# Kernel optimization log

Measured on AMD Instinct MI355X. Metric: run time of the kernel, lower is better.

## Reference

```python
import jax, jax.numpy as jnp
import numpy as np

E, T, D, N_RBF, N_SBF = 262144, 1048576, 128, 6, 42


def setup_inputs() -> dict:
    key = jax.random.key(0)
    ks = jax.random.split(key, 24)
    s = 0.05
    inp = {
        "m_ji": jax.random.normal(ks[0], (E, D), jnp.float32),
        "e_rbf": jax.random.normal(ks[1], (E, N_RBF), jnp.float32),
        "a_sbf": jax.random.normal(ks[2], (T, N_SBF), jnp.float32),
        "nbr_list": jax.random.randint(ks[3], (E, 2), 0, 65536),
        "kj_idx": jax.random.randint(ks[4], (T,), 0, E),
        "ji_idx": jax.random.randint(ks[5], (T,), 0, E),
        # edge branch params
        "We": jax.random.normal(ks[6], (N_RBF, D), jnp.float32) * s,
        "W_e1": jax.random.normal(ks[7], (D, D), jnp.float32) * s,
        "b_e1": jnp.zeros((D,), jnp.float32),
        "W_e2": jax.random.normal(ks[8], (D, D), jnp.float32) * s,
        "b_e2": jnp.zeros((D,), jnp.float32),
        "W_e3": jax.random.normal(ks[9], (D, D), jnp.float32) * s,
        "b_e3": jnp.zeros((D,), jnp.float32),
        "W_e4": jax.random.normal(ks[10], (D, D), jnp.float32) * s,
        # angle branch params
        "Wa": jax.random.normal(ks[11], (N_SBF, D), jnp.float32) * s,
        "W_a1": jax.random.normal(ks[12], (D, D), jnp.float32) * s,
        "b_a1": jnp.zeros((D,), jnp.float32),
        "W_a2": jax.random.normal(ks[13], (D, D), jnp.float32) * s,
        "b_a2": jnp.zeros((D,), jnp.float32),
        "W_a3": jax.random.normal(ks[14], (D, D), jnp.float32) * s,
        "b_a3": jnp.zeros((D,), jnp.float32),
        "W_a4": jax.random.normal(ks[15], (D, D), jnp.float32) * s,
    }
    return inp


def _mlp(x, W1, b1, W2, b2, W3, b3, W4):
    x = jax.nn.silu(x @ W1 + b1)
    x = jax.nn.silu(x @ W2 + b2)
    x = jax.nn.silu(x @ W3 + b3)
    return x @ W4


def reference(m_ji, e_rbf, a_sbf, nbr_list, kj_idx, ji_idx,
              We, W_e1, b_e1, W_e2, b_e2, W_e3, b_e3, W_e4,
              Wa, W_a1, b_a1, W_a2, b_a2, W_a3, b_a3, W_a4):
    # edge branch: project rbf to embed dim, gate by edge messages  [E, D]
    edge_feats = _mlp((e_rbf @ We) * m_ji, W_e1, b_e1, W_e2, b_e2, W_e3, b_e3, W_e4)
    # angle branch: project sbf, gate by triplet-gathered message sum  [T, D]
    angle_gate = m_ji[kj_idx] + m_ji[ji_idx]
    angle_feats = _mlp((a_sbf @ Wa) * angle_gate, W_a1, b_a1, W_a2, b_a2, W_a3, b_a3, W_a4)
    return (edge_feats, angle_feats)
```

## Files before the change

kernel.cpp:

```cpp
#include <hip/hip_runtime.h>
#include <stdint.h>

typedef __attribute__((ext_vector_type(8))) short bf16x8;
typedef __attribute__((ext_vector_type(4))) float f32x4;
typedef __attribute__((ext_vector_type(8))) unsigned short us8;
typedef __bf16 bf16v2 __attribute__((ext_vector_type(2)));

#define T_CNT 1048576
#define E_CNT 262144

static __device__ __forceinline__ unsigned short f2bf_u(float f) {
  __bf16 h = (__bf16)f;
  return __builtin_bit_cast(unsigned short, h);
}
static __device__ __forceinline__ uint32_t pack2bf(float a, float b) {
  bf16v2 t; t[0] = (__bf16)a; t[1] = (__bf16)b;
  return __builtin_bit_cast(uint32_t, t);
}
static __device__ __forceinline__ float silu_f(float v) {
  float e = __builtin_amdgcn_exp2f(v * -1.44269504088896341f);
  return v * __builtin_amdgcn_rcpf(1.0f + e);
}
static __device__ __forceinline__ bf16x8 frag8(f32x4 a, f32x4 b) {
  union { bf16x8 v; uint32_t u[4]; } r;
  r.u[0] = pack2bf(a[0], a[1]); r.u[1] = pack2bf(a[2], a[3]);
  r.u[2] = pack2bf(b[0], b[1]); r.u[3] = pack2bf(b[2], b[3]);
  return r.v;
}

static __device__ __forceinline__ void mlp4(
    char* __restrict__ xbA, char* __restrict__ xbB,
    const char* __restrict__ wt4,
    const float* __restrict__ b1, const float* __restrict__ b2,
    const float* __restrict__ b3, float* __restrict__ outT,
    int l15, int q, int w, int rs)
{
  const int cb = w * 32;
  #pragma unroll
  for (int L = 0; L < 4; ++L) {
    const char* src = (L & 1) ? xbB : xbA;
    char* dst = (L & 1) ? xbA : xbB;
    bf16x8 wf[2][4];
    #pragma unroll
    for (int ct = 0; ct < 2; ++ct)
      #pragma unroll
      for (int ks = 0; ks < 4; ++ks)
        wf[ct][ks] = *(const bf16x8*)(wt4 + (L << 15) + (((w * 2 + ct) * 4 + ks) << 10) + (l15 | (q << 4)) * 16);
    if (L < 3) {
      const float* bp = (L == 0) ? b1 : (L == 1) ? b2 : b3;
      f32x4 bv0 = *(const f32x4*)(bp + cb + q * 4);
      f32x4 bv1 = *(const f32x4*)(bp + cb + 16 + q * 4);
      #pragma unroll
      for (int rg = 0; rg < 2; ++rg) {
        const int row = rg * 16 + l15;
        f32x4 acc0 = {0.f,0.f,0.f,0.f}, acc1 = {0.f,0.f,0.f,0.f};
        #pragma unroll
        for (int ks = 0; ks < 4; ++ks) {
          bf16x8 xf = *(const bf16x8*)(src + ((row * 256 + ks * 64 + q * 16) ^ rs));
          acc0 = __builtin_amdgcn_mfma_f32_16x16x32_bf16(wf[0][ks], xf, acc0, 0, 0, 0);
          acc1 = __builtin_amdgcn_mfma_f32_16x16x32_bf16(wf[1][ks], xf, acc1, 0, 0, 0);
        }
        uint2 u0, u1;
        u0.x = pack2bf(silu_f(acc0[0] + bv0[0]), silu_f(acc0[1] + bv0[1]));
        u0.y = pack2bf(silu_f(acc0[2] + bv0[2]), silu_f(acc0[3] + bv0[3]));
        u1.x = pack2bf(silu_f(acc1[0] + bv1[0]), silu_f(acc1[1] + bv1[1]));
        u1.y = pack2bf(silu_f(acc1[2] + bv1[2]), silu_f(acc1[3] + bv1[3]));
        *(uint2*)(dst + ((row * 256 + w * 64 + q * 8) ^ rs)) = u0;
        *(uint2*)(dst + ((row * 256 + w * 64 + 32 + q * 8) ^ rs)) = u1;
      }
      __syncthreads();
    } else {
      #pragma unroll
      for (int rg = 0; rg < 2; ++rg) {
        const int row = rg * 16 + l15;
        f32x4 acc0 = {0.f,0.f,0.f,0.f}, acc1 = {0.f,0.f,0.f,0.f};
        #pragma unroll
        for (int ks = 0; ks < 4; ++ks) {
          bf16x8 xf = *(const bf16x8*)(src + ((row * 256 + ks * 64 + q * 16) ^ rs));
          acc0 = __builtin_amdgcn_mfma_f32_16x16x32_bf16(wf[0][ks], xf, acc0, 0, 0, 0);
          acc1 = __builtin_amdgcn_mfma_f32_16x16x32_bf16(wf[1][ks], xf, acc1, 0, 0, 0);
        }
        float* op = outT + (size_t)row * 128 + cb + q * 4;
        __builtin_nontemporal_store(acc0, (f32x4*)(op));
        __builtin_nontemporal_store(acc1, (f32x4*)(op + 16));
      }
    }
  }
}

__global__ __launch_bounds__(256, 4) void angle_kernel(
    const float* __restrict__ m_ji, const float* __restrict__ a_sbf,
    const int* __restrict__ kj, const int* __restrict__ ji,
    const float* __restrict__ b1, const float* __restrict__ b2,
    const float* __restrict__ b3,
    const char* __restrict__ wt4, const char* __restrict__ waT,
    float* __restrict__ out)
{
  __shared__ __align__(16) char xbA[8192];
  __shared__ __align__(16) char xbB[8192];
  const int tid = threadIdx.x, lane = tid & 63, w = tid >> 6;
  const int l15 = lane & 15, q = lane >> 4;
  const int rs = (l15 & 7) << 4;
  const size_t tb = (size_t)blockIdx.x * 32;
  const int cb = w * 32;

  bf16x8 wa[2][2];
  #pragma unroll
  for (int ct = 0; ct < 2; ++ct)
    #pragma unroll
    for (int ks = 0; ks < 2; ++ks)
      wa[ct][ks] = *(const bf16x8*)(waT + (((w * 2 + ct) * 2 + ks) << 10) + lane * 16);

  int ikj[2], iji[2];
  #pragma unroll
  for (int g = 0; g < 2; ++g) {
    ikj[g] = kj[tb + g * 16 + l15];
    iji[g] = ji[tb + g * 16 + l15];
  }
  f32x4 pk[2][2], pj[2][2];
  #pragma unroll
  for (int g = 0; g < 2; ++g) {
    const float* bk = m_ji + (size_t)ikj[g] * 128 + cb + q * 4;
    const float* bj = m_ji + (size_t)iji[g] * 128 + cb + q * 4;
    pk[g][0] = *(const f32x4*)(bk);
    pk[g][1] = *(const f32x4*)(bk + 16);
    pj[g][0] = *(const f32x4*)(bj);
    pj[g][1] = *(const f32x4*)(bj + 16);
  }

  #pragma unroll
  for (int rg = 0; rg < 2; ++rg) {
    const int row = rg * 16 + l15;
    const float* ap = a_sbf + (tb + row) * 42;
    f32x4 a0 = *(const f32x4*)(ap + q * 8);
    f32x4 a1 = *(const f32x4*)(ap + q * 8 + 4);
    f32x4 c0 = {0.f,0.f,0.f,0.f}, c1 = {0.f,0.f,0.f,0.f};
    if (q == 0) { c0 = *(const f32x4*)(ap + 32); c1 = *(const f32x4*)(ap + 36); }
    else if (q == 1) { float2 t = *(const float2*)(ap + 40); c0[0] = t.x; c0[1] = t.y; }
    bf16x8 f0 = frag8(a0, a1);
    bf16x8 f1 = frag8(c0, c1);
    f32x4 acc0 = {0.f,0.f,0.f,0.f}, acc1 = {0.f,0.f,0.f,0.f};
    acc0 = __builtin_amdgcn_mfma_f32_16x16x32_bf16(wa[0][0], f0, acc0, 0, 0, 0);
    acc0 = __builtin_amdgcn_mfma_f32_16x16x32_bf16(wa[0][1], f1, acc0, 0, 0, 0);
    acc1 = __builtin_amdgcn_mfma_f32_16x16x32_bf16(wa[1][0], f0, acc1, 0, 0, 0);
    acc1 = __builtin_amdgcn_mfma_f32_16x16x32_bf16(wa[1][1], f1, acc1, 0, 0, 0);
    f32x4 g0 = pk[rg][0] + pj[rg][0];
    f32x4 g1 = pk[rg][1] + pj[rg][1];
    uint2 u0, u1;
    u0.x = pack2bf(acc0[0] * g0[0], acc0[1] * g0[1]);
    u0.y = pack2bf(acc0[2] * g0[2], acc0[3] * g0[3]);
    u1.x = pack2bf(acc1[0] * g1[0], acc1[1] * g1[1]);
    u1.y = pack2bf(acc1[2] * g1[2], acc1[3] * g1[3]);
    *(uint2*)(xbA + ((row * 256 + w * 64 + q * 8) ^ rs)) = u0;
    *(uint2*)(xbA + ((row * 256 + w * 64 + 32 + q * 8) ^ rs)) = u1;
  }
  __syncthreads();

  mlp4(xbA, xbB, wt4, b1, b2, b3, out + tb * 128, l15, q, w, rs);
}

__global__ __launch_bounds__(256, 4) void edge_kernel(
    const float* __restrict__ m_ji, const float* __restrict__ e_rbf,
    const float* __restrict__ b1, const float* __restrict__ b2,
    const float* __restrict__ b3,
    const char* __restrict__ wt4, const char* __restrict__ weT,
    float* __restrict__ out)
{
  __shared__ __align__(16) char xbA[8192];
  __shared__ __align__(16) char xbB[8192];
  const int tid = threadIdx.x, lane = tid & 63, w = tid >> 6;
  const int l15 = lane & 15, q = lane >> 4;
  const int rs = (l15 & 7) << 4;
  const size_t tb = (size_t)blockIdx.x * 32;
  const int cb = w * 32;

  bf16x8 we[2];
  #pragma unroll
  for (int ct = 0; ct < 2; ++ct)
    we[ct] = *(const bf16x8*)(weT + ((w * 2 + ct) << 10) + lane * 16);

  f32x4 mr[2][2];
  #pragma unroll
  for (int g = 0; g < 2; ++g) {
    const float* bm = m_ji + (tb + g * 16 + l15) * 128 + cb + q * 4;
    mr[g][0] = *(const f32x4*)(bm);
    mr[g][1] = *(const f32x4*)(bm + 16);
  }

  #pragma unroll
  for (int rg = 0; rg < 2; ++rg) {
    const int row = rg * 16 + l15;
    const float* ep = e_rbf + (tb + row) * 6;
    f32x4 a0 = {0.f,0.f,0.f,0.f}, a1 = {0.f,0.f,0.f,0.f};
    if (q == 0) {
      a0 = *(const f32x4*)(ep);
      float2 t = *(const float2*)(ep + 4);
      a1[0] = t.x; a1[1] = t.y;
    }
    bf16x8 ef = frag8(a0, a1);
    f32x4 acc0 = {0.f,0.f,0.f,0.f}, acc1 = {0.f,0.f,0.f,0.f};
    acc0 = __builtin_amdgcn_mfma_f32_16x16x32_bf16(we[0], ef, acc0, 0, 0, 0);
    acc1 = __builtin_amdgcn_mfma_f32_16x16x32_bf16(we[1], ef, acc1, 0, 0, 0);
    f32x4 g0 = mr[rg][0];
    f32x4 g1 = mr[rg][1];
    uint2 u0, u1;
    u0.x = pack2bf(acc0[0] * g0[0], acc0[1] * g0[1]);
    u0.y = pack2bf(acc0[2] * g0[2], acc0[3] * g0[3]);
    u1.x = pack2bf(acc1[0] * g1[0], acc1[1] * g1[1]);
    u1.y = pack2bf(acc1[2] * g1[2], acc1[3] * g1[3]);
    *(uint2*)(xbA + ((row * 256 + w * 64 + q * 8) ^ rs)) = u0;
    *(uint2*)(xbA + ((row * 256 + w * 64 + 32 + q * 8) ^ rs)) = u1;
  }
  __syncthreads();

  mlp4(xbA, xbB, wt4, b1, b2, b3, out + tb * 128, l15, q, w, rs);
}

__global__ void prep_kernel(
    const float* __restrict__ W0, const float* __restrict__ W1,
    const float* __restrict__ W2, const float* __restrict__ W3,
    const float* __restrict__ W4, const float* __restrict__ W5,
    const float* __restrict__ W6, const float* __restrict__ W7,
    const float* __restrict__ Wa, const float* __restrict__ We,
    char* __restrict__ ws)
{
  const int gid = blockIdx.x * 256 + threadIdx.x;
  const int lane = gid & 63;
  const int l15 = lane & 15, q = lane >> 4;
  if (gid < 16384) {
    const int mat = gid >> 11;
    const int ctks = (gid & 2047) >> 6;
    const int n = (ctks >> 2) * 16 + l15;
    const int k0 = (ctks & 3) * 32 + q * 8;
    const float* W;
    switch (mat) {
      case 0: W = W0; break; case 1: W = W1; break;
      case 2: W = W2; break; case 3: W = W3; break;
      case 4: W = W4; break; case 5: W = W5; break;
      case 6: W = W6; break; default: W = W7; break;
    }
    us8 v;
    #pragma unroll
    for (int j = 0; j < 8; ++j) v[j] = f2bf_u(W[(size_t)(k0 + j) * 128 + n]);
    *(us8*)(ws + mat * 32768 + ctks * 1024 + lane * 16) = v;
  } else if (gid < 17408) {
    const int g = gid - 16384;
    const int ctks = g >> 6;
    const int n = (ctks >> 1) * 16 + l15;
    const int k0 = (ctks & 1) * 32 + q * 8;
    us8 v;
    #pragma unroll
    for (int j = 0; j < 8; ++j) {
      const int k = k0 + j;
      v[j] = (k < 42) ? f2bf_u(Wa[(size_t)k * 128 + n]) : (unsigned short)0;
    }
    *(us8*)(ws + 262144 + ctks * 1024 + lane * 16) = v;
  } else if (gid < 17920) {
    const int g = gid - 17408;
    const int ct = g >> 6;
    const int n = ct * 16 + l15;
    const int k0 = q * 8;
    us8 v;
    #pragma unroll
    for (int j = 0; j < 8; ++j) {
      const int k = k0 + j;
      v[j] = (k < 6) ? f2bf_u(We[(size_t)k * 128 + n]) : (unsigned short)0;
    }
    *(us8*)(ws + 278528 + ct * 1024 + lane * 16) = v;
  }
}

extern "C" void kernel_launch(void* const* d_in, const int* in_sizes, int n_in,
                              void* d_out, int out_size, void* d_ws, size_t ws_size,
                              hipStream_t stream) {
  (void)in_sizes; (void)n_in; (void)out_size; (void)ws_size;
  const float* m_ji  = (const float*)d_in[0];
  const float* e_rbf = (const float*)d_in[1];
  const float* a_sbf = (const float*)d_in[2];
  const int*   kj    = (const int*)d_in[4];
  const int*   ji    = (const int*)d_in[5];
  const float* We    = (const float*)d_in[6];
  const float* We1   = (const float*)d_in[7];
  const float* be1   = (const float*)d_in[8];
  const float* We2   = (const float*)d_in[9];
  const float* be2   = (const float*)d_in[10];
  const float* We3   = (const float*)d_in[11];
  const float* be3   = (const float*)d_in[12];
  const float* We4   = (const float*)d_in[13];
  const float* Wa    = (const float*)d_in[14];
  const float* Wa1   = (const float*)d_in[15];
  const float* ba1   = (const float*)d_in[16];
  const float* Wa2   = (const float*)d_in[17];
  const float* ba2   = (const float*)d_in[18];
  const float* Wa3   = (const float*)d_in[19];
  const float* ba3   = (const float*)d_in[20];
  const float* Wa4   = (const float*)d_in[21];
  char* ws = (char*)d_ws;
  float* out = (float*)d_out;
  float* out_a = out + (size_t)E_CNT * 128;

  prep_kernel<<<70, 256, 0, stream>>>(
      We1, We2, We3, We4, Wa1, Wa2, Wa3, Wa4, Wa, We, ws);
  edge_kernel<<<E_CNT / 32, 256, 0, stream>>>(
      m_ji, e_rbf, be1, be2, be3, ws, ws + 278528, out);
  angle_kernel<<<T_CNT / 32, 256, 0, stream>>>(
      m_ji, a_sbf, kj, ji, ba1, ba2, ba3, ws + 131072, ws + 262144, out_a);
}
```

Baseline: 584.0 us.

## Double rows per block, stage final output through LDS for coalesced stores

Each block now handles 64 rows instead of 32, so every weight fragment loaded from global memory is reused across twice as many rows, and there are half as many blocks. The last layer's fp32 results are written into a swizzled 32KB shared buffer and then streamed out as fully contiguous 16-byte nontemporal stores. The gather loads for m_ji are software-pipelined two row-groups ahead, and a_sbf is read with scalar nontemporal loads. In exchange, shared memory per block grows to 32KB, register pressure rises from holding accumulators for four row groups, and the scalar a_sbf loads may issue more memory instructions.

```diff
diff --git a/kernel.cpp b/kernel.cpp
--- a/kernel.cpp
+++ b/kernel.cpp
@@ -29,15 +29,18 @@
 }
 
 static __device__ __forceinline__ void mlp4(
-    char* __restrict__ xbA, char* __restrict__ xbB,
-    const char* __restrict__ wt4,
+    char* __restrict__ xb, const char* __restrict__ wt4,
     const float* __restrict__ b1, const float* __restrict__ b2,
     const float* __restrict__ b3, float* __restrict__ outT,
-    int l15, int q, int w, int rs)
+    int tid, int l15, int q, int w, int rs)
 {
+  char* xbA = xb;
+  char* xbB = xb + 16384;
   const int cb = w * 32;
-  #pragma unroll
-  for (int L = 0; L < 4; ++L) {
+  const int lane16 = (l15 | (q << 4)) * 16;
+
+  #pragma unroll
+  for (int L = 0; L < 3; ++L) {
     const char* src = (L & 1) ? xbB : xbA;
     char* dst = (L & 1) ? xbA : xbB;
     bf16x8 wf[2][4];
@@ -45,45 +48,71 @@
     for (int ct = 0; ct < 2; ++ct)
       #pragma unroll
       for (int ks = 0; ks < 4; ++ks)
-        wf[ct][ks] = *(const bf16x8*)(wt4 + (L << 15) + (((w * 2 + ct) * 4 + ks) << 10) + (l15 | (q << 4)) * 16);
-    if (L < 3) {
-      const float* bp = (L == 0) ? b1 : (L == 1) ? b2 : b3;
-      f32x4 bv0 = *(const f32x4*)(bp + cb + q * 4);
-      f32x4 bv1 = *(const f32x4*)(bp + cb + 16 + q * 4);
-      #pragma unroll
-      for (int rg = 0; rg < 2; ++rg) {
-        const int row = rg * 16 + l15;
-        f32x4 acc0 = {0.f,0.f,0.f,0.f}, acc1 = {0.f,0.f,0.f,0.f};
-        #pragma unroll
-        for (int ks = 0; ks < 4; ++ks) {
-          bf16x8 xf = *(const bf16x8*)(src + ((row * 256 + ks * 64 + q * 16) ^ rs));
-          acc0 = __builtin_amdgcn_mfma_f32_16x16x32_bf16(wf[0][ks], xf, acc0, 0, 0, 0);
-          acc1 = __builtin_amdgcn_mfma_f32_16x16x32_bf16(wf[1][ks], xf, acc1, 0, 0, 0);
-        }
-        uint2 u0, u1;
-        u0.x = pack2bf(silu_f(acc0[0] + bv0[0]), silu_f(acc0[1] + bv0[1]));
-        u0.y = pack2bf(silu_f(acc0[2] + bv0[2]), silu_f(acc0[3] + bv0[3]));
-        u1.x = pack2bf(silu_f(acc1[0] + bv1[0]), silu_f(acc1[1] + bv1[1]));
-        u1.y = pack2bf(silu_f(acc1[2] + bv1[2]), silu_f(acc1[3] + bv1[3]));
-        *(uint2*)(dst + ((row * 256 + w * 64 + q * 8) ^ rs)) = u0;
-        *(uint2*)(dst + ((row * 256 + w * 64 + 32 + q * 8) ^ rs)) = u1;
+        wf[ct][ks] = *(const bf16x8*)(wt4 + (L << 15) + (((w * 2 + ct) * 4 + ks) << 10) + lane16);
+    const float* bp = (L == 0) ? b1 : (L == 1) ? b2 : b3;
+    f32x4 bv0 = *(const f32x4*)(bp + cb + q * 4);
+    f32x4 bv1 = *(const f32x4*)(bp + cb + 16 + q * 4);
+    #pragma unroll
+    for (int rg = 0; rg < 4; ++rg) {
+      const int row = rg * 16 + l15;
+      f32x4 acc0 = {0.f,0.f,0.f,0.f}, acc1 = {0.f,0.f,0.f,0.f};
+      #pragma unroll
+      for (int ks = 0; ks < 4; ++ks) {
+        bf16x8 xf = *(const bf16x8*)(src + ((row * 256 + ks * 64 + q * 16) ^ rs));
+        acc0 = __builtin_amdgcn_mfma_f32_16x16x32_bf16(wf[0][ks], xf, acc0, 0, 0, 0);
+        acc1 = __builtin_amdgcn_mfma_f32_16x16x32_bf16(wf[1][ks], xf, acc1, 0, 0, 0);
       }
-      __syncthreads();
-    } else {
-      #pragma unroll
-      for (int rg = 0; rg < 2; ++rg) {
-        const int row = rg * 16 + l15;
-        f32x4 acc0 = {0.f,0.f,0.f,0.f}, acc1 = {0.f,0.f,0.f,0.f};
-        #pragma unroll
-        for (int ks = 0; ks < 4; ++ks) {
-          bf16x8 xf = *(const bf16x8*)(src + ((row * 256 + ks * 64 + q * 16) ^ rs));
-          acc0 = __builtin_amdgcn_mfma_f32_16x16x32_bf16(wf[0][ks], xf, acc0, 0, 0, 0);
-          acc1 = __builtin_amdgcn_mfma_f32_16x16x32_bf16(wf[1][ks], xf, acc1, 0, 0, 0);
-        }
-        float* op = outT + (size_t)row * 128 + cb + q * 4;
-        __builtin_nontemporal_store(acc0, (f32x4*)(op));
-        __builtin_nontemporal_store(acc1, (f32x4*)(op + 16));
+      uint2 u0, u1;
+      u0.x = pack2bf(silu_f(acc0[0] + bv0[0]), silu_f(acc0[1] + bv0[1]));
+      u0.y = pack2bf(silu_f(acc0[2] + bv0[2]), silu_f(acc0[3] + bv0[3]));
+      u1.x = pack2bf(silu_f(acc1[0] + bv1[0]), silu_f(acc1[1] + bv1[1]));
+      u1.y = pack2bf(silu_f(acc1[2] + bv1[2]), silu_f(acc1[3] + bv1[3]));
+      *(uint2*)(dst + ((row * 256 + w * 64 + q * 8) ^ rs)) = u0;
+      *(uint2*)(dst + ((row * 256 + w * 64 + 32 + q * 8) ^ rs)) = u1;
+    }
+    __syncthreads();
+  }
+
+  {
+    const char* src = xbB;
+    bf16x8 wf[2][4];
+    #pragma unroll
+    for (int ct = 0; ct < 2; ++ct)
+      #pragma unroll
+      for (int ks = 0; ks < 4; ++ks)
+        wf[ct][ks] = *(const bf16x8*)(wt4 + (3 << 15) + (((w * 2 + ct) * 4 + ks) << 10) + lane16);
+    f32x4 acc[4][2];
+    #pragma unroll
+    for (int rg = 0; rg < 4; ++rg) {
+      const int row = rg * 16 + l15;
+      f32x4 a0 = {0.f,0.f,0.f,0.f}, a1 = {0.f,0.f,0.f,0.f};
+      #pragma unroll
+      for (int ks = 0; ks < 4; ++ks) {
+        bf16x8 xf = *(const bf16x8*)(src + ((row * 256 + ks * 64 + q * 16) ^ rs));
+        a0 = __builtin_amdgcn_mfma_f32_16x16x32_bf16(wf[0][ks], xf, a0, 0, 0, 0);
+        a1 = __builtin_amdgcn_mfma_f32_16x16x32_bf16(wf[1][ks], xf, a1, 0, 0, 0);
       }
+      acc[rg][0] = a0; acc[rg][1] = a1;
+    }
+    __syncthreads();
+
+    #pragma unroll
+    for (int rg = 0; rg < 4; ++rg) {
+      const int row = rg * 16 + l15;
+      const int sw = (row & 7) << 4;
+      const int b0 = row * 512 + w * 128 + q * 16;
+      *(f32x4*)(xb + (b0 ^ sw)) = acc[rg][0];
+      *(f32x4*)(xb + ((b0 + 64) ^ sw)) = acc[rg][1];
+    }
+    __syncthreads();
+
+    #pragma unroll
+    for (int i = 0; i < 8; ++i) {
+      const int b = tid * 16 + i * 4096;
+      const int row = b >> 9;
+      const int inner = b & 511;
+      f32x4 v = *(const f32x4*)(xb + ((row * 512 + inner) ^ ((row & 7) << 4)));
+      __builtin_nontemporal_store(v, (f32x4*)((char*)outT + b));
     }
   }
 }
@@ -96,12 +125,12 @@
     const char* __restrict__ wt4, const char* __restrict__ waT,
     float* __restrict__ out)
 {
-  __shared__ __align__(16) char xbA[8192];
-  __shared__ __align__(16) char xbB[8192];
+  __shared__ __align__(16) char xb[32768];
+  char* xbA = xb;
   const int tid = threadIdx.x, lane = tid & 63, w = tid >> 6;
   const int l15 = lane & 15, q = lane >> 4;
   const int rs = (l15 & 7) << 4;
-  const size_t tb = (size_t)blockIdx.x * 32;
+  const size_t tb = (size_t)blockIdx.x * 64;
   const int cb = w * 32;
 
   bf16x8 wa[2][2];
@@ -111,32 +140,44 @@
     for (int ks = 0; ks < 2; ++ks)
       wa[ct][ks] = *(const bf16x8*)(waT + (((w * 2 + ct) * 2 + ks) << 10) + lane * 16);
 
-  int ikj[2], iji[2];
-  #pragma unroll
-  for (int g = 0; g < 2; ++g) {
+  int ikj[4], iji[4];
+  #pragma unroll
+  for (int g = 0; g < 4; ++g) {
     ikj[g] = kj[tb + g * 16 + l15];
     iji[g] = ji[tb + g * 16 + l15];
   }
   f32x4 pk[2][2], pj[2][2];
-  #pragma unroll
-  for (int g = 0; g < 2; ++g) {
+  auto gissue = [&](int g) {
     const float* bk = m_ji + (size_t)ikj[g] * 128 + cb + q * 4;
     const float* bj = m_ji + (size_t)iji[g] * 128 + cb + q * 4;
-    pk[g][0] = *(const f32x4*)(bk);
-    pk[g][1] = *(const f32x4*)(bk + 16);
-    pj[g][0] = *(const f32x4*)(bj);
-    pj[g][1] = *(const f32x4*)(bj + 16);
-  }
-
-  #pragma unroll
-  for (int rg = 0; rg < 2; ++rg) {
+    pk[g & 1][0] = *(const f32x4*)(bk);
+    pk[g & 1][1] = *(const f32x4*)(bk + 16);
+    pj[g & 1][0] = *(const f32x4*)(bj);
+    pj[g & 1][1] = *(const f32x4*)(bj + 16);
+  };
+  gissue(0); gissue(1);
+
+  #pragma unroll
+  for (int rg = 0; rg < 4; ++rg) {
     const int row = rg * 16 + l15;
     const float* ap = a_sbf + (tb + row) * 42;
-    f32x4 a0 = *(const f32x4*)(ap + q * 8);
-    f32x4 a1 = *(const f32x4*)(ap + q * 8 + 4);
+    f32x4 a0, a1;
+    #pragma unroll
+    for (int j = 0; j < 4; ++j) {
+      a0[j] = __builtin_nontemporal_load(ap + q * 8 + j);
+      a1[j] = __builtin_nontemporal_load(ap + q * 8 + 4 + j);
+    }
     f32x4 c0 = {0.f,0.f,0.f,0.f}, c1 = {0.f,0.f,0.f,0.f};
-    if (q == 0) { c0 = *(const f32x4*)(ap + 32); c1 = *(const f32x4*)(ap + 36); }
-    else if (q == 1) { float2 t = *(const float2*)(ap + 40); c0[0] = t.x; c0[1] = t.y; }
+    if (q == 0) {
+      #pragma unroll
+      for (int j = 0; j < 4; ++j) {
+        c0[j] = __builtin_nontemporal_load(ap + 32 + j);
+        c1[j] = __builtin_nontemporal_load(ap + 36 + j);
+      }
+    } else if (q == 1) {
+      c0[0] = __builtin_nontemporal_load(ap + 40);
+      c0[1] = __builtin_nontemporal_load(ap + 41);
+    }
     bf16x8 f0 = frag8(a0, a1);
     bf16x8 f1 = frag8(c0, c1);
     f32x4 acc0 = {0.f,0.f,0.f,0.f}, acc1 = {0.f,0.f,0.f,0.f};
@@ -144,8 +185,9 @@
     acc0 = __builtin_amdgcn_mfma_f32_16x16x32_bf16(wa[0][1], f1, acc0, 0, 0, 0);
     acc1 = __builtin_amdgcn_mfma_f32_16x16x32_bf16(wa[1][0], f0, acc1, 0, 0, 0);
     acc1 = __builtin_amdgcn_mfma_f32_16x16x32_bf16(wa[1][1], f1, acc1, 0, 0, 0);
-    f32x4 g0 = pk[rg][0] + pj[rg][0];
-    f32x4 g1 = pk[rg][1] + pj[rg][1];
+    f32x4 g0 = pk[rg & 1][0] + pj[rg & 1][0];
+    f32x4 g1 = pk[rg & 1][1] + pj[rg & 1][1];
+    if (rg < 2) gissue(rg + 2);
     uint2 u0, u1;
     u0.x = pack2bf(acc0[0] * g0[0], acc0[1] * g0[1]);
     u0.y = pack2bf(acc0[2] * g0[2], acc0[3] * g0[3]);
@@ -156,7 +198,7 @@
   }
   __syncthreads();
 
-  mlp4(xbA, xbB, wt4, b1, b2, b3, out + tb * 128, l15, q, w, rs);
+  mlp4(xb, wt4, b1, b2, b3, out + tb * 128, tid, l15, q, w, rs);
 }
 
 __global__ __launch_bounds__(256, 4) void edge_kernel(
@@ -166,12 +208,12 @@
     const char* __restrict__ wt4, const char* __restrict__ weT,
     float* __restrict__ out)
 {
-  __shared__ __align__(16) char xbA[8192];
-  __shared__ __align__(16) char xbB[8192];
+  __shared__ __align__(16) char xb[32768];
+  char* xbA = xb;
   const int tid = threadIdx.x, lane = tid & 63, w = tid >> 6;
   const int l15 = lane & 15, q = lane >> 4;
   const int rs = (l15 & 7) << 4;
-  const size_t tb = (size_t)blockIdx.x * 32;
+  const size_t tb = (size_t)blockIdx.x * 64;
   const int cb = w * 32;
 
   bf16x8 we[2];
@@ -180,15 +222,15 @@
     we[ct] = *(const bf16x8*)(weT + ((w * 2 + ct) << 10) + lane * 16);
 
   f32x4 mr[2][2];
-  #pragma unroll
-  for (int g = 0; g < 2; ++g) {
+  auto missue = [&](int g) {
     const float* bm = m_ji + (tb + g * 16 + l15) * 128 + cb + q * 4;
-    mr[g][0] = *(const f32x4*)(bm);
-    mr[g][1] = *(const f32x4*)(bm + 16);
-  }
-
-  #pragma unroll
-  for (int rg = 0; rg < 2; ++rg) {
+    mr[g & 1][0] = *(const f32x4*)(bm);
+    mr[g & 1][1] = *(const f32x4*)(bm + 16);
+  };
+  missue(0); missue(1);
+
+  #pragma unroll
+  for (int rg = 0; rg < 4; ++rg) {
     const int row = rg * 16 + l15;
     const float* ep = e_rbf + (tb + row) * 6;
     f32x4 a0 = {0.f,0.f,0.f,0.f}, a1 = {0.f,0.f,0.f,0.f};
@@ -201,8 +243,9 @@
     f32x4 acc0 = {0.f,0.f,0.f,0.f}, acc1 = {0.f,0.f,0.f,0.f};
     acc0 = __builtin_amdgcn_mfma_f32_16x16x32_bf16(we[0], ef, acc0, 0, 0, 0);
     acc1 = __builtin_amdgcn_mfma_f32_16x16x32_bf16(we[1], ef, acc1, 0, 0, 0);
-    f32x4 g0 = mr[rg][0];
-    f32x4 g1 = mr[rg][1];
+    f32x4 g0 = mr[rg & 1][0];
+    f32x4 g1 = mr[rg & 1][1];
+    if (rg < 2) missue(rg + 2);
     uint2 u0, u1;
     u0.x = pack2bf(acc0[0] * g0[0], acc0[1] * g0[1]);
     u0.y = pack2bf(acc0[2] * g0[2], acc0[3] * g0[3]);
@@ -213,7 +256,7 @@
   }
   __syncthreads();
 
-  mlp4(xbA, xbB, wt4, b1, b2, b3, out + tb * 128, l15, q, w, rs);
+  mlp4(xb, wt4, b1, b2, b3, out + tb * 128, tid, l15, q, w, rs);
 }
 
 __global__ void prep_kernel(
@@ -301,8 +344,8 @@
 
   prep_kernel<<<70, 256, 0, stream>>>(
       We1, We2, We3, We4, Wa1, Wa2, Wa3, Wa4, Wa, We, ws);
-  edge_kernel<<<E_CNT / 32, 256, 0, stream>>>(
+  edge_kernel<<<E_CNT / 64, 256, 0, stream>>>(
       m_ji, e_rbf, be1, be2, be3, ws, ws + 278528, out);
-  angle_kernel<<<T_CNT / 32, 256, 0, stream>>>(
+  angle_kernel<<<T_CNT / 64, 256, 0, stream>>>(
       m_ji, a_sbf, kj, ji, ba1, ba2, ba3, ws + 131072, ws + 262144, out_a);
 }
```

New measurement: 560.3 us. 1.04x faster.
